# Optimization experiments

Measured on AMD Instinct MI355X. Metric: run time of the kernel, lower is better.

## Reference

```python
import jax, jax.numpy as jnp
import numpy as np

N_KERNELS = 21
N_LAYERS = 2
N_HEADS = 8
ATT_DIM = 32
FF_HID = 100
EMB = 300


def kernel_mus(n):
    mus = [1.0]
    bin_size = 2.0 / (n - 1)
    mus.append(1.0 - bin_size / 2.0)
    for _ in range(1, n - 1):
        mus.append(mus[-1] - bin_size)
    return np.array(mus, dtype=np.float32)


def kernel_sigmas(n):
    return np.array([0.001] + [0.1] * (n - 1), dtype=np.float32)


def setup_inputs() -> dict:
    key = jax.random.key(0)
    ks = jax.random.split(key, 12)
    B, LQ, LD = 32, 64, 512
    u = lambda k, s, a: jax.random.uniform(k, s, jnp.float32, -a, a)
    return dict(
        q_embed=jax.random.normal(ks[0], (B, LQ, EMB), jnp.float32),
        d_embed=jax.random.normal(ks[1], (B, LD, EMB), jnp.float32),
        mask_q=(jax.random.uniform(ks[2], (B, LQ)) > 0.1).astype(jnp.float32),
        mask_d=(jax.random.uniform(ks[3], (B, LD)) > 0.1).astype(jnp.float32),
        mixer=jnp.full((1, 1, 1), 0.5, jnp.float32),
        nn_scaler=jnp.full((1,), 0.01, jnp.float32),
        ff_w1=u(ks[4], (N_LAYERS, EMB, FF_HID), 0.05),
        ff_b1=jnp.zeros((N_LAYERS, FF_HID), jnp.float32),
        ff_w2=u(ks[5], (N_LAYERS, FF_HID, EMB), 0.05),
        ff_b2=jnp.zeros((N_LAYERS, EMB), jnp.float32),
        ln1_g=jnp.ones((N_LAYERS, EMB), jnp.float32),
        ln1_b=jnp.zeros((N_LAYERS, EMB), jnp.float32),
        att_w=u(ks[6], (N_LAYERS, EMB, 3 * ATT_DIM), 0.05),
        att_b=jnp.zeros((N_LAYERS, 3 * ATT_DIM), jnp.float32),
        out_w=u(ks[7], (N_LAYERS, ATT_DIM, EMB), 0.05),
        out_b=jnp.zeros((N_LAYERS, EMB), jnp.float32),
        ln2_g=jnp.ones((N_LAYERS, EMB), jnp.float32),
        ln2_b=jnp.zeros((N_LAYERS, EMB), jnp.float32),
        dense_w=u(ks[8], (1, N_KERNELS), 0.014),
    )


def _layer_norm(x, g, b, eps=1e-6):
    m = jnp.mean(x, -1, keepdims=True)
    s = jnp.std(x, -1, keepdims=True, ddof=1)  # torch std is unbiased
    return g * (x - m) / (s + eps) + b


def _encoder(x, mask, p):
    # AllenNLP StackedSelfAttentionEncoder: [FF -> res+LN -> MHSA -> res+LN] x2
    B, T, E = x.shape
    scale = jnp.sqrt(jnp.float32(E // N_HEADS))
    hd = ATT_DIM // N_HEADS
    for l in range(N_LAYERS):
        h = jax.nn.relu(x @ p['ff_w1'][l] + p['ff_b1'][l]) @ p['ff_w2'][l] + p['ff_b2'][l]
        h = _layer_norm(h + x, p['ln1_g'][l], p['ln1_b'][l])
        c = h @ p['att_w'][l] + p['att_b'][l]              # [B,T,3*ATT_DIM]
        q = c[..., :ATT_DIM].reshape(B, T, N_HEADS, hd)
        k = c[..., ATT_DIM:2 * ATT_DIM].reshape(B, T, N_HEADS, hd)
        v = c[..., 2 * ATT_DIM:].reshape(B, T, N_HEADS, hd)
        sims = jnp.einsum('bqhd,bkhd->bhqk', q / scale, k)
        m = mask[:, None, None, :]
        att = jax.nn.softmax(sims * m, axis=-1) * m         # AllenNLP masked_softmax
        att = att / (jnp.sum(att, -1, keepdims=True) + 1e-13)
        o = jnp.einsum('bhqk,bkhd->bqhd', att, v).reshape(B, T, ATT_DIM)
        o = o @ p['out_w'][l] + p['out_b'][l]
        x = _layer_norm(o + h, p['ln2_g'][l], p['ln2_b'][l])
    return x


def reference(q_embed, d_embed, mask_q, mask_d, mixer, nn_scaler,
              ff_w1, ff_b1, ff_w2, ff_b2, ln1_g, ln1_b,
              att_w, att_b, out_w, out_b, ln2_g, ln2_b, dense_w):
    p = dict(ff_w1=ff_w1, ff_b1=ff_b1, ff_w2=ff_w2, ff_b2=ff_b2,
             ln1_g=ln1_g, ln1_b=ln1_b, att_w=att_w, att_b=att_b,
             out_w=out_w, out_b=out_b, ln2_g=ln2_g, ln2_b=ln2_b)
    mu = jnp.asarray(kernel_mus(N_KERNELS))        # [K]
    sigma = jnp.asarray(kernel_sigmas(N_KERNELS))  # [K]
    mq = mask_q[..., None]
    md = mask_d[..., None]
    q = q_embed * mq
    d = d_embed * md
    qc = _encoder(q, mask_q, p)
    dc = _encoder(d, mask_d, p)
    q = (mixer * q + (1.0 - mixer) * qc) * mq
    d = (mixer * d + (1.0 - mixer) * dc) * md
    qd_mask = mask_q[:, :, None] * mask_d[:, None, :]  # [B,Q,D]
    qn = q / (jnp.linalg.norm(q, axis=-1, keepdims=True) + 1e-13)
    dn = d / (jnp.linalg.norm(d, axis=-1, keepdims=True) + 1e-13)
    cos = jnp.einsum('bqe,bde->bqd', qn, dn) * qd_mask
    # Gaussian RBF soft histogram: [B,Q,D,K]
    kr = jnp.exp(-(cos[..., None] - mu) ** 2 / (2.0 * sigma ** 2)) * qd_mask[..., None]
    pkq = jnp.sum(kr, axis=2)                                 # [B,Q,K]
    log_pkq = jnp.log2(jnp.clip(pkq, 1e-10)) * nn_scaler
    per_kernel = jnp.sum(log_pkq * mq, axis=1)                # [B,K]
    return jnp.squeeze(per_kernel @ dense_w.T, axis=1)        # [B]
```

## Files before the change

kernel.cpp:

```cpp
#include <hip/hip_runtime.h>
#include <hip/hip_bf16.h>

#define BATCH 32
#define LQ 64
#define LD 512
#define EMB 300
#define FFH 100
#define ATTD 32
#define NH 8
#define NK 21
#define MQ (BATCH * LQ)
#define MD (BATCH * LD)
#define MALL (MQ + MD)

typedef __attribute__((ext_vector_type(8))) short bf16x8;
typedef __attribute__((ext_vector_type(4))) float f32x4;

__device__ __forceinline__ float wave_sum(float v) {
    #pragma unroll
    for (int off = 32; off > 0; off >>= 1) v += __shfl_xor(v, off);
    return v;
}

__device__ __forceinline__ float bf2f(__hip_bfloat16 h) {
    return __bfloat162float(h);
}

__device__ __forceinline__ float4 bf4_to_f4(const __hip_bfloat16* p) {
    uint2 u = *(const uint2*)p;
    float4 f;
    f.x = __uint_as_float((u.x & 0xffffu) << 16);
    f.y = __uint_as_float(u.x & 0xffff0000u);
    f.z = __uint_as_float((u.y & 0xffffu) << 16);
    f.w = __uint_as_float(u.y & 0xffff0000u);
    return f;
}

__global__ void maskmul_all(const float* __restrict__ q_embed, const float* __restrict__ d_embed,
                            const float* __restrict__ mask_q, const float* __restrict__ mask_d,
                            __hip_bfloat16* __restrict__ xbf, float* __restrict__ mall) {
    int i = blockIdx.x * blockDim.x + threadIdx.x;
    if (i >= MALL * EMB) return;
    int tok = i / EMB;
    float m, v;
    if (tok < MQ) {
        m = mask_q[tok];
        v = q_embed[i];
    } else {
        m = mask_d[tok - MQ];
        v = d_embed[i - MQ * EMB];
    }
    xbf[i] = __float2bfloat16(v * m);
    if (i % EMB == 0) mall[tok] = m;
}

__device__ __forceinline__ void conv_seg(const float* __restrict__ w, __hip_bfloat16* __restrict__ wt,
                                         int j, int K, int N) {
    int l = j / (K * N);
    int r = j % (K * N);
    int k = r / N, n = r % N;
    wt[(size_t)l * N * K + (size_t)n * K + k] = __float2bfloat16(w[j]);
}
__global__ void convert_all(const float* __restrict__ w1, const float* __restrict__ w2,
                            const float* __restrict__ aw, const float* __restrict__ ow,
                            __hip_bfloat16* __restrict__ w1t, __hip_bfloat16* __restrict__ w2t,
                            __hip_bfloat16* __restrict__ awt, __hip_bfloat16* __restrict__ owt) {
    int i = blockIdx.x * blockDim.x + threadIdx.x;
    const int S1 = 2 * EMB * FFH;
    const int S2 = S1 + 2 * FFH * EMB;
    const int S3 = S2 + 2 * EMB * 96;
    const int S4 = S3 + 2 * ATTD * EMB;
    if (i < S1)       conv_seg(w1, w1t, i, EMB, FFH);
    else if (i < S2)  conv_seg(w2, w2t, i - S1, FFH, EMB);
    else if (i < S3)  conv_seg(aw, awt, i - S2, EMB, 96);
    else if (i < S4)  conv_seg(ow, owt, i - S3, ATTD, EMB);
}

__device__ __forceinline__ void stage_row8(const __hip_bfloat16* __restrict__ src, bool rowvalid,
                                           int K, int gk, __hip_bfloat16* dst) {
    if (rowvalid && gk + 8 <= K) {
        const uint2* p = (const uint2*)(src + gk);
        uint2 a = p[0], b = p[1];
        *(uint2*)dst = a;
        *(uint2*)(dst + 4) = b;
    } else {
        #pragma unroll
        for (int j = 0; j < 8; j++)
            dst[j] = (rowvalid && gk + j < K) ? src[gk + j] : __float2bfloat16(0.f);
    }
}

template <bool RELU>
__global__ __launch_bounds__(256) void gemm_mfma(const __hip_bfloat16* __restrict__ A,
                                                 const __hip_bfloat16* __restrict__ Bt,
                                                 const float* __restrict__ bias,
                                                 __hip_bfloat16* __restrict__ Cb,
                                                 int M, int N, int K) {
    __shared__ __align__(16) __hip_bfloat16 As[64][40];
    __shared__ __align__(16) __hip_bfloat16 Bs[64][40];
    const int tid = threadIdx.x;
    const int m0 = blockIdx.y * 64, n0 = blockIdx.x * 64;
    const int lane = tid & 63;
    const int wv = tid >> 6;
    const int wm = wv >> 1, wn = wv & 1;
    const int l15 = lane & 15, lg = lane >> 4;
    const int srow = tid >> 2, sk8 = (tid & 3) * 8;
    f32x4 acc[2][2] = {};
    const int NS = (K + 31) >> 5;
    const __hip_bfloat16* arow = A + (size_t)(m0 + srow) * K;
    const bool bvalid = (n0 + srow) < N;
    const __hip_bfloat16* brow = Bt + (size_t)(n0 + srow) * K;

    for (int s = 0; s < NS; s++) {
        const int gk = (s << 5) + sk8;
        if (s) __syncthreads();
        stage_row8(arow, true, K, gk, &As[srow][sk8]);
        stage_row8(brow, bvalid, K, gk, &Bs[srow][sk8]);
        __syncthreads();
        bf16x8 af0 = *(const bf16x8*)&As[wm * 32 + l15][lg * 8];
        bf16x8 af1 = *(const bf16x8*)&As[wm * 32 + 16 + l15][lg * 8];
        bf16x8 bf0 = *(const bf16x8*)&Bs[wn * 32 + l15][lg * 8];
        bf16x8 bf1 = *(const bf16x8*)&Bs[wn * 32 + 16 + l15][lg * 8];
        acc[0][0] = __builtin_amdgcn_mfma_f32_16x16x32_bf16(af0, bf0, acc[0][0], 0, 0, 0);
        acc[0][1] = __builtin_amdgcn_mfma_f32_16x16x32_bf16(af0, bf1, acc[0][1], 0, 0, 0);
        acc[1][0] = __builtin_amdgcn_mfma_f32_16x16x32_bf16(af1, bf0, acc[1][0], 0, 0, 0);
        acc[1][1] = __builtin_amdgcn_mfma_f32_16x16x32_bf16(af1, bf1, acc[1][1], 0, 0, 0);
    }

    #pragma unroll
    for (int fc = 0; fc < 2; fc++) {
        int col = n0 + wn * 32 + fc * 16 + l15;
        if (col >= N) continue;
        float bs = bias[col];
        #pragma unroll
        for (int fr = 0; fr < 2; fr++) {
            int rbase = m0 + wm * 32 + fr * 16 + lg * 4;
            #pragma unroll
            for (int r = 0; r < 4; r++) {
                int row = rbase + r;
                float v = acc[fr][fc][r] + bs;
                if (RELU) v = fmaxf(v, 0.f);
                Cb[(size_t)row * N + col] = __float2bfloat16(v);
            }
        }
    }
}

__global__ __launch_bounds__(256) void gemm_ln(const __hip_bfloat16* __restrict__ A,
                                               const __hip_bfloat16* __restrict__ Bt,
                                               const float* __restrict__ bias,
                                               const __hip_bfloat16* __restrict__ Res,
                                               const float* __restrict__ g,
                                               const float* __restrict__ beta,
                                               __hip_bfloat16* __restrict__ Y,
                                               int M, int K) {
    __shared__ __align__(16) __hip_bfloat16 As[32][40];
    __shared__ __align__(16) __hip_bfloat16 Bs[320][40];
    __shared__ float red[2][4][32];
    const int tid = threadIdx.x;
    const int m0 = blockIdx.x * 32;
    const int lane = tid & 63;
    const int wv = tid >> 6;
    const int l15 = lane & 15, lg = lane >> 4;
    const int c0 = wv * 80;
    f32x4 acc[2][5] = {};
    const int NS = (K + 31) >> 5;

    for (int s = 0; s < NS; s++) {
        const int gk0 = s << 5;
        if (s) __syncthreads();
        for (int ch = tid; ch < 1408; ch += 256) {
            if (ch < 128) {
                int row = ch >> 2, k8 = (ch & 3) * 8;
                stage_row8(A + (size_t)(m0 + row) * K, true, K, gk0 + k8, &As[row][k8]);
            } else {
                int cc = ch - 128;
                int row = cc >> 2, k8 = (cc & 3) * 8;
                stage_row8(Bt + (size_t)row * K, row < EMB, K, gk0 + k8, &Bs[row][k8]);
            }
        }
        __syncthreads();
        bf16x8 af[2], bfr[5];
        af[0] = *(const bf16x8*)&As[l15][lg * 8];
        af[1] = *(const bf16x8*)&As[16 + l15][lg * 8];
        #pragma unroll
        for (int fc = 0; fc < 5; fc++)
            bfr[fc] = *(const bf16x8*)&Bs[c0 + fc * 16 + l15][lg * 8];
        #pragma unroll
        for (int fr = 0; fr < 2; fr++)
            #pragma unroll
            for (int fc = 0; fc < 5; fc++)
                acc[fr][fc] = __builtin_amdgcn_mfma_f32_16x16x32_bf16(af[fr], bfr[fc], acc[fr][fc], 0, 0, 0);
    }

    float rs[2][4];
    #pragma unroll
    for (int fr = 0; fr < 2; fr++)
        #pragma unroll
        for (int r = 0; r < 4; r++) rs[fr][r] = 0.f;
    #pragma unroll
    for (int fc = 0; fc < 5; fc++) {
        int col = c0 + fc * 16 + l15;
        bool valid = col < EMB;
        float bs = valid ? bias[col] : 0.f;
        #pragma unroll
        for (int fr = 0; fr < 2; fr++) {
            int rowb = m0 + fr * 16 + lg * 4;
            #pragma unroll
            for (int r = 0; r < 4; r++) {
                float v = 0.f;
                if (valid) v = acc[fr][fc][r] + bs + bf2f(Res[(size_t)(rowb + r) * EMB + col]);
                acc[fr][fc][r] = v;
                rs[fr][r] += v;
            }
        }
    }
    #pragma unroll
    for (int fr = 0; fr < 2; fr++)
        #pragma unroll
        for (int r = 0; r < 4; r++)
            #pragma unroll
            for (int off = 1; off < 16; off <<= 1)
                rs[fr][r] += __shfl_xor(rs[fr][r], off);
    if (l15 == 0) {
        #pragma unroll
        for (int fr = 0; fr < 2; fr++)
            #pragma unroll
            for (int r = 0; r < 4; r++)
                red[0][wv][fr * 16 + lg * 4 + r] = rs[fr][r];
    }
    __syncthreads();
    float mean[2][4];
    #pragma unroll
    for (int fr = 0; fr < 2; fr++)
        #pragma unroll
        for (int r = 0; r < 4; r++) {
            int ri = fr * 16 + lg * 4 + r;
            mean[fr][r] = (red[0][0][ri] + red[0][1][ri] + red[0][2][ri] + red[0][3][ri]) * (1.f / EMB);
        }
    float rq[2][4];
    #pragma unroll
    for (int fr = 0; fr < 2; fr++)
        #pragma unroll
        for (int r = 0; r < 4; r++) rq[fr][r] = 0.f;
    #pragma unroll
    for (int fc = 0; fc < 5; fc++) {
        int col = c0 + fc * 16 + l15;
        bool valid = col < EMB;
        #pragma unroll
        for (int fr = 0; fr < 2; fr++)
            #pragma unroll
            for (int r = 0; r < 4; r++) {
                if (valid) {
                    float d = acc[fr][fc][r] - mean[fr][r];
                    rq[fr][r] += d * d;
                }
            }
    }
    #pragma unroll
    for (int fr = 0; fr < 2; fr++)
        #pragma unroll
        for (int r = 0; r < 4; r++)
            #pragma unroll
            for (int off = 1; off < 16; off <<= 1)
                rq[fr][r] += __shfl_xor(rq[fr][r], off);
    if (l15 == 0) {
        #pragma unroll
        for (int fr = 0; fr < 2; fr++)
            #pragma unroll
            for (int r = 0; r < 4; r++)
                red[1][wv][fr * 16 + lg * 4 + r] = rq[fr][r];
    }
    __syncthreads();
    float inv[2][4];
    #pragma unroll
    for (int fr = 0; fr < 2; fr++)
        #pragma unroll
        for (int r = 0; r < 4; r++) {
            int ri = fr * 16 + lg * 4 + r;
            float tot = red[1][0][ri] + red[1][1][ri] + red[1][2][ri] + red[1][3][ri];
            float stdv = sqrtf(tot * (1.f / (EMB - 1)));
            inv[fr][r] = 1.f / (stdv + 1e-6f);
        }
    #pragma unroll
    for (int fc = 0; fc < 5; fc++) {
        int col = c0 + fc * 16 + l15;
        if (col >= EMB) continue;
        float gv = g[col], bv = beta[col];
        #pragma unroll
        for (int fr = 0; fr < 2; fr++) {
            int rowb = m0 + fr * 16 + lg * 4;
            #pragma unroll
            for (int r = 0; r < 4; r++) {
                float y = gv * (acc[fr][fc][r] - mean[fr][r]) * inv[fr][r] + bv;
                Y[(size_t)(rowb + r) * EMB + col] = __float2bfloat16(y);
            }
        }
    }
}

template <int T, int RPB, int KS>
__device__ __forceinline__ void attn_body(const __hip_bfloat16* __restrict__ cseg,
                                          const float* __restrict__ mask,
                                          __hip_bfloat16* __restrict__ oseg,
                                          int bh, int rb, char* smem) {
    constexpr int BLK = 512;
    float4* Ks = (float4*)smem;
    float4* Vs = Ks + T;
    float* part = (float*)(Vs + T);
    float* nmask_s = part + RPB * 5 * (KS - 1);
    const int b = bh / NH, h = bh % NH;
    const int tid = threadIdx.x;
    const __hip_bfloat16* base = cseg + (size_t)b * T * 96;

    if (tid == 0) *nmask_s = 0.f;
    __syncthreads();
    float lnm = 0.f;
    for (int j = tid; j < T; j += BLK) {
        float m = mask[b * T + j];
        float4 kv = bf4_to_f4(base + (size_t)j * 96 + ATTD + h * 4);
        float4 vv = bf4_to_f4(base + (size_t)j * 96 + 2 * ATTD + h * 4);
        kv.x *= m; kv.y *= m; kv.z *= m; kv.w *= m;
        vv.x *= m; vv.y *= m; vv.z *= m; vv.w *= m;
        Ks[j] = kv;
        Vs[j] = vv;
        lnm += 1.f - m;
    }
    lnm = wave_sum(lnm);
    if ((tid & 63) == 0 && lnm != 0.f) atomicAdd(nmask_s, lnm);
    __syncthreads();

    const int r = rb * RPB + (tid % RPB);
    const int ks = tid / RPB;
    const float inv_scale = 0.16439898730535729f;
    float4 qv = bf4_to_f4(base + (size_t)r * 96 + h * 4);
    qv.x *= inv_scale; qv.y *= inv_scale; qv.z *= inv_scale; qv.w *= inv_scale;

    float Sall = 0.f, ox = 0.f, oy = 0.f, oz = 0.f, ow = 0.f;
    constexpr int KC = T / KS;
    const int k0 = ks * KC;
    #pragma unroll 4
    for (int k = k0; k < k0 + KC; k++) {
        float4 kv = Ks[k];
        float4 vv = Vs[k];
        float s = fmaf(qv.x, kv.x, fmaf(qv.y, kv.y, fmaf(qv.z, kv.z, qv.w * kv.w)));
        float e = __expf(s);
        Sall += e;
        ox = fmaf(e, vv.x, ox);
        oy = fmaf(e, vv.y, oy);
        oz = fmaf(e, vv.z, oz);
        ow = fmaf(e, vv.w, ow);
    }
    if (ks > 0) {
        float* p = &part[((ks - 1) * RPB + (tid % RPB)) * 5];
        p[0] = Sall; p[1] = ox; p[2] = oy; p[3] = oz; p[4] = ow;
    }
    __syncthreads();
    if (ks == 0) {
        #pragma unroll
        for (int s2 = 0; s2 < KS - 1; s2++) {
            const float* p = &part[(s2 * RPB + r - rb * RPB) * 5];
            Sall += p[0]; ox += p[1]; oy += p[2]; oz += p[3]; ow += p[4];
        }
        float Sm = Sall - *nmask_s;
        float inv = 1.f / (Sm + 1e-13f * Sall);
        __hip_bfloat16* op = oseg + (size_t)(b * T + r) * ATTD + h * 4;
        op[0] = __float2bfloat16(ox * inv);
        op[1] = __float2bfloat16(oy * inv);
        op[2] = __float2bfloat16(oz * inv);
        op[3] = __float2bfloat16(ow * inv);
    }
}

__global__ __launch_bounds__(512) void attn_both(const __hip_bfloat16* __restrict__ cbf,
                                                 const float* __restrict__ mask_q,
                                                 const float* __restrict__ mask_d,
                                                 __hip_bfloat16* __restrict__ o32) {
    __shared__ __align__(16) char smem[24576];
    int blk = blockIdx.x;
    if (blk < BATCH * NH) {
        attn_body<LQ, 64, 8>(cbf, mask_q, o32, blk, 0, smem);
    } else {
        int bid = blk - BATCH * NH;
        attn_body<LD, 128, 4>(cbf + (size_t)MQ * 96, mask_d, o32 + (size_t)MQ * ATTD,
                              bid >> 2, bid & 3, smem);
    }
}

__global__ __launch_bounds__(256) void cos_mfma(const __hip_bfloat16* __restrict__ Qn,
                                                const __hip_bfloat16* __restrict__ Dn,
                                                float* __restrict__ Cos) {
    __shared__ __align__(16) __hip_bfloat16 As[64][40];
    __shared__ __align__(16) __hip_bfloat16 Bs[64][40];
    const int b = blockIdx.y;
    const int n0 = blockIdx.x * 64;
    const int tid = threadIdx.x;
    const int lane = tid & 63;
    const int wv = tid >> 6;
    const int wm = wv >> 1, wn = wv & 1;
    const int l15 = lane & 15, lg = lane >> 4;
    const int srow = tid >> 2, sk8 = (tid & 3) * 8;
    f32x4 acc[2][2] = {};
    const int NS = (EMB + 31) >> 5;
    const __hip_bfloat16* arow = Qn + ((size_t)b * LQ + srow) * EMB;
    const __hip_bfloat16* brow = Dn + ((size_t)b * LD + n0 + srow) * EMB;

    for (int s = 0; s < NS; s++) {
        const int gk = (s << 5) + sk8;
        if (s) __syncthreads();
        stage_row8(arow, true, EMB, gk, &As[srow][sk8]);
        stage_row8(brow, true, EMB, gk, &Bs[srow][sk8]);
        __syncthreads();
        bf16x8 af0 = *(const bf16x8*)&As[wm * 32 + l15][lg * 8];
        bf16x8 af1 = *(const bf16x8*)&As[wm * 32 + 16 + l15][lg * 8];
        bf16x8 bf0 = *(const bf16x8*)&Bs[wn * 32 + l15][lg * 8];
        bf16x8 bf1 = *(const bf16x8*)&Bs[wn * 32 + 16 + l15][lg * 8];
        acc[0][0] = __builtin_amdgcn_mfma_f32_16x16x32_bf16(af0, bf0, acc[0][0], 0, 0, 0);
        acc[0][1] = __builtin_amdgcn_mfma_f32_16x16x32_bf16(af0, bf1, acc[0][1], 0, 0, 0);
        acc[1][0] = __builtin_amdgcn_mfma_f32_16x16x32_bf16(af1, bf0, acc[1][0], 0, 0, 0);
        acc[1][1] = __builtin_amdgcn_mfma_f32_16x16x32_bf16(af1, bf1, acc[1][1], 0, 0, 0);
    }

    float* cb = Cos + (size_t)b * LQ * LD;
    #pragma unroll
    for (int fc = 0; fc < 2; fc++) {
        int col = n0 + wn * 32 + fc * 16 + l15;
        #pragma unroll
        for (int fr = 0; fr < 2; fr++) {
            int rbase = wm * 32 + fr * 16 + lg * 4;
            #pragma unroll
            for (int r = 0; r < 4; r++) {
                cb[(size_t)(rbase + r) * LD + col] = acc[fr][fc][r];
            }
        }
    }
}

__global__ __launch_bounds__(256) void mixnorm_bf(const __hip_bfloat16* __restrict__ x,
                                                  const __hip_bfloat16* __restrict__ xc,
                                                  const float* __restrict__ mask,
                                                  const float* __restrict__ mixer,
                                                  __hip_bfloat16* __restrict__ out) {
    int wid = (blockIdx.x * 256 + threadIdx.x) >> 6;
    int lane = threadIdx.x & 63;
    float mixv = mixer[0];
    float mval = mask[wid];
    const __hip_bfloat16* xr = x + (size_t)wid * EMB;
    const __hip_bfloat16* xcr = xc + (size_t)wid * EMB;
    float v[5];
    float s2 = 0.f;
    #pragma unroll
    for (int r = 0; r < 5; r++) {
        int idx = lane + r * 64;
        float val = 0.f;
        if (idx < EMB) val = (mixv * bf2f(xr[idx]) + (1.f - mixv) * bf2f(xcr[idx])) * mval;
        v[r] = val;
        s2 += val * val;
    }
    s2 = wave_sum(s2);
    float inv = 1.f / (sqrtf(s2) + 1e-13f);
    __hip_bfloat16* o = out + (size_t)wid * EMB;
    #pragma unroll
    for (int r = 0; r < 5; r++) {
        int idx = lane + r * 64;
        if (idx < EMB) o[idx] = __float2bfloat16(v[r] * inv);
    }
}

__global__ __launch_bounds__(256) void pool_kernel(const float* __restrict__ Cos,
                                                   const float* __restrict__ mask_q,
                                                   const float* __restrict__ mask_d,
                                                   const float* __restrict__ nn_scaler,
                                                   float* __restrict__ lp) {
    int wid = (blockIdx.x * 256 + threadIdx.x) >> 6;
    int lane = threadIdx.x & 63;
    int b = wid >> 6, qi = wid & 63;
    const float* crow = Cos + ((size_t)b * LQ + qi) * LD;
    const float* md = mask_d + b * LD;
    float acc[NK];
    #pragma unroll
    for (int k = 0; k < NK; k++) acc[k] = 0.f;
    #pragma unroll
    for (int rr = 0; rr < LD / 64; rr++) {
        int dj = rr * 64 + lane;
        float m = md[dj];
        if (m != 0.f) {
            float cv = crow[dj];
            float d0 = cv - 1.0f;
            acc[0] += __expf(d0 * d0 * -500000.0f);
            #pragma unroll
            for (int g = 0; g < 4; g++) {
                float mu_a = 0.95f - 0.5f * g;
                float dc = cv - mu_a;
                float t = __expf(dc * dc * -50.0f);
                float r = __expf(fmaf(-10.0f, dc, -0.5f));
                #pragma unroll
                for (int j = 0; j < 5; j++) {
                    acc[1 + 5 * g + j] += t;
                    t *= r;
                    r *= 0.36787944117144233f;
                }
            }
        }
    }
    float mq = mask_q[b * LQ + qi];
    float ns = nn_scaler[0];
    #pragma unroll
    for (int k = 0; k < NK; k++) {
        float s = wave_sum(acc[k]);
        if (lane == 0) lp[((size_t)b * LQ + qi) * NK + k] = log2f(fmaxf(s, 1e-10f)) * ns * mq;
    }
}

__global__ void final_kernel(const float* __restrict__ lp, const float* __restrict__ dense_w,
                             float* __restrict__ out) {
    int b = blockIdx.x;
    int t = threadIdx.x;
    float s = 0.f;
    if (t < NK) {
        for (int qi = 0; qi < LQ; qi++) s += lp[((size_t)b * LQ + qi) * NK + t];
        s *= dense_w[t];
    }
    s = wave_sum(s);
    if (t == 0) out[b] = s;
}

extern "C" void kernel_launch(void* const* d_in, const int* in_sizes, int n_in,
                              void* d_out, int out_size, void* d_ws, size_t ws_size,
                              hipStream_t stream) {
    (void)in_sizes; (void)n_in; (void)out_size; (void)ws_size;
    const float* q_embed  = (const float*)d_in[0];
    const float* d_embed  = (const float*)d_in[1];
    const float* mask_q   = (const float*)d_in[2];
    const float* mask_d   = (const float*)d_in[3];
    const float* mixer    = (const float*)d_in[4];
    const float* nn_scaler= (const float*)d_in[5];
    const float* ff_w1    = (const float*)d_in[6];
    const float* ff_b1    = (const float*)d_in[7];
    const float* ff_w2    = (const float*)d_in[8];
    const float* ff_b2    = (const float*)d_in[9];
    const float* ln1_g    = (const float*)d_in[10];
    const float* ln1_b    = (const float*)d_in[11];
    const float* att_w    = (const float*)d_in[12];
    const float* att_b    = (const float*)d_in[13];
    const float* out_w    = (const float*)d_in[14];
    const float* out_b    = (const float*)d_in[15];
    const float* ln2_g    = (const float*)d_in[16];
    const float* ln2_b    = (const float*)d_in[17];
    const float* dense_w  = (const float*)d_in[18];
    float* out = (float*)d_out;

    float* ws   = (float*)d_ws;
    float* cosb = ws;
    float* lp   = cosb + 1048576;
    float* mall = lp + 43008;
    __hip_bfloat16* xbf   = (__hip_bfloat16*)(mall + MALL);
    __hip_bfloat16* xcbf  = xbf  + (size_t)MALL * EMB;
    __hip_bfloat16* xc2bf = xcbf + (size_t)MALL * EMB;
    __hip_bfloat16* hbf   = xc2bf + (size_t)MALL * EMB;
    __hip_bfloat16* t1bf  = hbf  + (size_t)MALL * EMB;
    __hip_bfloat16* cbf   = t1bf + (size_t)MALL * FFH;
    __hip_bfloat16* o32bf = cbf  + (size_t)MALL * 96;
    __hip_bfloat16* w1t   = o32bf + (size_t)MALL * ATTD;
    __hip_bfloat16* w2t   = w1t + 2 * FFH * EMB;
    __hip_bfloat16* awt   = w2t + 2 * EMB * FFH;
    __hip_bfloat16* owt   = awt + 2 * 96 * EMB;

    convert_all<<<(196800 + 255) / 256, 256, 0, stream>>>(ff_w1, ff_w2, att_w, out_w,
                                                          w1t, w2t, awt, owt);
    maskmul_all<<<(MALL * EMB + 255) / 256, 256, 0, stream>>>(q_embed, d_embed, mask_q, mask_d,
                                                              xbf, mall);

    const __hip_bfloat16* xcur = xbf;
    for (int l = 0; l < 2; l++) {
        __hip_bfloat16* xout = (l == 0) ? xcbf : xc2bf;
        gemm_mfma<true><<<dim3(2, MALL / 64), 256, 0, stream>>>(
            xcur, w1t + (size_t)l * FFH * EMB, ff_b1 + l * FFH, t1bf, MALL, FFH, EMB);
        gemm_ln<<<MALL / 32, 256, 0, stream>>>(
            t1bf, w2t + (size_t)l * EMB * FFH, ff_b2 + l * EMB, xcur,
            ln1_g + l * EMB, ln1_b + l * EMB, hbf, MALL, FFH);
        gemm_mfma<false><<<dim3(2, MALL / 64), 256, 0, stream>>>(
            hbf, awt + (size_t)l * 96 * EMB, att_b + l * 96, cbf, MALL, 96, EMB);
        attn_both<<<BATCH * NH + BATCH * NH * (LD / 128), 512, 0, stream>>>(
            cbf, mask_q, mask_d, o32bf);
        gemm_ln<<<MALL / 32, 256, 0, stream>>>(
            o32bf, owt + (size_t)l * EMB * ATTD, out_b + l * EMB, hbf,
            ln2_g + l * EMB, ln2_b + l * EMB, xout, MALL, ATTD);
        xcur = xout;
    }

    mixnorm_bf<<<MALL / 4, 256, 0, stream>>>(xbf, xc2bf, mall, mixer, hbf);

    cos_mfma<<<dim3(LD / 64, BATCH), 256, 0, stream>>>(hbf, hbf + (size_t)MQ * EMB, cosb);

    pool_kernel<<<(BATCH * LQ) / 4, 256, 0, stream>>>(cosb, mask_q, mask_d, nn_scaler, lp);

    final_kernel<<<BATCH, 64, 0, stream>>>(lp, dense_w, out);
}
```

Baseline: 242.5 us.

## Enlarge gemm_ln row tile to 64 and split-K the cosine GEMM

The fused GEMM+LayerNorm kernel now processes 64 rows per block instead of 32, so the 300-column weight tile staged in shared memory is reused across twice as many rows and half as many blocks are launched. The cosine-similarity GEMM is split into two K halves along a new grid dimension, each writing a separate partial buffer. The pooling kernel sums the two partials as it reads them. This raises parallelism for the small cos GEMM (256 blocks to 512) at the cost of doubled cos write/read traffic, and the gemm_ln change raises register pressure while reducing block count.

```diff
diff --git a/kernel.cpp b/kernel.cpp
--- a/kernel.cpp
+++ b/kernel.cpp
@@ -154,48 +154,50 @@
                                                const float* __restrict__ beta,
                                                __hip_bfloat16* __restrict__ Y,
                                                int M, int K) {
-    __shared__ __align__(16) __hip_bfloat16 As[32][40];
+    __shared__ __align__(16) __hip_bfloat16 As[64][40];
     __shared__ __align__(16) __hip_bfloat16 Bs[320][40];
-    __shared__ float red[2][4][32];
+    __shared__ float red[2][4][64];
     const int tid = threadIdx.x;
-    const int m0 = blockIdx.x * 32;
+    const int m0 = blockIdx.x * 64;
     const int lane = tid & 63;
     const int wv = tid >> 6;
     const int l15 = lane & 15, lg = lane >> 4;
     const int c0 = wv * 80;
-    f32x4 acc[2][5] = {};
+    f32x4 acc[4][5] = {};
     const int NS = (K + 31) >> 5;
 
     for (int s = 0; s < NS; s++) {
         const int gk0 = s << 5;
         if (s) __syncthreads();
-        for (int ch = tid; ch < 1408; ch += 256) {
-            if (ch < 128) {
+        #pragma unroll
+        for (int rnd = 0; rnd < 6; rnd++) {
+            int ch = tid + rnd * 256;
+            if (ch < 256) {
                 int row = ch >> 2, k8 = (ch & 3) * 8;
                 stage_row8(A + (size_t)(m0 + row) * K, true, K, gk0 + k8, &As[row][k8]);
             } else {
-                int cc = ch - 128;
+                int cc = ch - 256;
                 int row = cc >> 2, k8 = (cc & 3) * 8;
                 stage_row8(Bt + (size_t)row * K, row < EMB, K, gk0 + k8, &Bs[row][k8]);
             }
         }
         __syncthreads();
-        bf16x8 af[2], bfr[5];
-        af[0] = *(const bf16x8*)&As[l15][lg * 8];
-        af[1] = *(const bf16x8*)&As[16 + l15][lg * 8];
+        bf16x8 bfr[5];
         #pragma unroll
         for (int fc = 0; fc < 5; fc++)
             bfr[fc] = *(const bf16x8*)&Bs[c0 + fc * 16 + l15][lg * 8];
         #pragma unroll
-        for (int fr = 0; fr < 2; fr++)
+        for (int fr = 0; fr < 4; fr++) {
+            bf16x8 af = *(const bf16x8*)&As[fr * 16 + l15][lg * 8];
             #pragma unroll
             for (int fc = 0; fc < 5; fc++)
-                acc[fr][fc] = __builtin_amdgcn_mfma_f32_16x16x32_bf16(af[fr], bfr[fc], acc[fr][fc], 0, 0, 0);
-    }
-
-    float rs[2][4];
-    #pragma unroll
-    for (int fr = 0; fr < 2; fr++)
+                acc[fr][fc] = __builtin_amdgcn_mfma_f32_16x16x32_bf16(af, bfr[fc], acc[fr][fc], 0, 0, 0);
+        }
+    }
+
+    float rs[4][4];
+    #pragma unroll
+    for (int fr = 0; fr < 4; fr++)
         #pragma unroll
         for (int r = 0; r < 4; r++) rs[fr][r] = 0.f;
     #pragma unroll
@@ -204,7 +206,7 @@
         bool valid = col < EMB;
         float bs = valid ? bias[col] : 0.f;
         #pragma unroll
-        for (int fr = 0; fr < 2; fr++) {
+        for (int fr = 0; fr < 4; fr++) {
             int rowb = m0 + fr * 16 + lg * 4;
             #pragma unroll
             for (int r = 0; r < 4; r++) {
@@ -216,7 +218,7 @@
         }
     }
     #pragma unroll
-    for (int fr = 0; fr < 2; fr++)
+    for (int fr = 0; fr < 4; fr++)
         #pragma unroll
         for (int r = 0; r < 4; r++)
             #pragma unroll
@@ -224,23 +226,23 @@
                 rs[fr][r] += __shfl_xor(rs[fr][r], off);
     if (l15 == 0) {
         #pragma unroll
-        for (int fr = 0; fr < 2; fr++)
+        for (int fr = 0; fr < 4; fr++)
             #pragma unroll
             for (int r = 0; r < 4; r++)
                 red[0][wv][fr * 16 + lg * 4 + r] = rs[fr][r];
     }
     __syncthreads();
-    float mean[2][4];
-    #pragma unroll
-    for (int fr = 0; fr < 2; fr++)
+    float mean[4][4];
+    #pragma unroll
+    for (int fr = 0; fr < 4; fr++)
         #pragma unroll
         for (int r = 0; r < 4; r++) {
             int ri = fr * 16 + lg * 4 + r;
             mean[fr][r] = (red[0][0][ri] + red[0][1][ri] + red[0][2][ri] + red[0][3][ri]) * (1.f / EMB);
         }
-    float rq[2][4];
-    #pragma unroll
-    for (int fr = 0; fr < 2; fr++)
+    float rq[4][4];
+    #pragma unroll
+    for (int fr = 0; fr < 4; fr++)
         #pragma unroll
         for (int r = 0; r < 4; r++) rq[fr][r] = 0.f;
     #pragma unroll
@@ -248,7 +250,7 @@
         int col = c0 + fc * 16 + l15;
         bool valid = col < EMB;
         #pragma unroll
-        for (int fr = 0; fr < 2; fr++)
+        for (int fr = 0; fr < 4; fr++)
             #pragma unroll
             for (int r = 0; r < 4; r++) {
                 if (valid) {
@@ -258,7 +260,7 @@
             }
     }
     #pragma unroll
-    for (int fr = 0; fr < 2; fr++)
+    for (int fr = 0; fr < 4; fr++)
         #pragma unroll
         for (int r = 0; r < 4; r++)
             #pragma unroll
@@ -266,34 +268,26 @@
                 rq[fr][r] += __shfl_xor(rq[fr][r], off);
     if (l15 == 0) {
         #pragma unroll
-        for (int fr = 0; fr < 2; fr++)
+        for (int fr = 0; fr < 4; fr++)
             #pragma unroll
             for (int r = 0; r < 4; r++)
                 red[1][wv][fr * 16 + lg * 4 + r] = rq[fr][r];
     }
     __syncthreads();
-    float inv[2][4];
-    #pragma unroll
-    for (int fr = 0; fr < 2; fr++)
+    #pragma unroll
+    for (int fr = 0; fr < 4; fr++) {
         #pragma unroll
         for (int r = 0; r < 4; r++) {
             int ri = fr * 16 + lg * 4 + r;
             float tot = red[1][0][ri] + red[1][1][ri] + red[1][2][ri] + red[1][3][ri];
             float stdv = sqrtf(tot * (1.f / (EMB - 1)));
-            inv[fr][r] = 1.f / (stdv + 1e-6f);
-        }
-    #pragma unroll
-    for (int fc = 0; fc < 5; fc++) {
-        int col = c0 + fc * 16 + l15;
-        if (col >= EMB) continue;
-        float gv = g[col], bv = beta[col];
-        #pragma unroll
-        for (int fr = 0; fr < 2; fr++) {
-            int rowb = m0 + fr * 16 + lg * 4;
-            #pragma unroll
-            for (int r = 0; r < 4; r++) {
-                float y = gv * (acc[fr][fc][r] - mean[fr][r]) * inv[fr][r] + bv;
-                Y[(size_t)(rowb + r) * EMB + col] = __float2bfloat16(y);
+            float invv = 1.f / (stdv + 1e-6f);
+            #pragma unroll
+            for (int fc = 0; fc < 5; fc++) {
+                int col = c0 + fc * 16 + l15;
+                if (col >= EMB) continue;
+                float y = g[col] * (acc[fr][fc][r] - mean[fr][r]) * invv + beta[col];
+                Y[(size_t)(m0 + fr * 16 + lg * 4 + r) * EMB + col] = __float2bfloat16(y);
             }
         }
     }
@@ -394,6 +388,8 @@
     __shared__ __align__(16) __hip_bfloat16 Bs[64][40];
     const int b = blockIdx.y;
     const int n0 = blockIdx.x * 64;
+    const int kh = blockIdx.z;
+    const int kbeg = kh * 160;
     const int tid = threadIdx.x;
     const int lane = tid & 63;
     const int wv = tid >> 6;
@@ -401,12 +397,11 @@
     const int l15 = lane & 15, lg = lane >> 4;
     const int srow = tid >> 2, sk8 = (tid & 3) * 8;
     f32x4 acc[2][2] = {};
-    const int NS = (EMB + 31) >> 5;
     const __hip_bfloat16* arow = Qn + ((size_t)b * LQ + srow) * EMB;
     const __hip_bfloat16* brow = Dn + ((size_t)b * LD + n0 + srow) * EMB;
 
-    for (int s = 0; s < NS; s++) {
-        const int gk = (s << 5) + sk8;
+    for (int s = 0; s < 5; s++) {
+        const int gk = kbeg + (s << 5) + sk8;
         if (s) __syncthreads();
         stage_row8(arow, true, EMB, gk, &As[srow][sk8]);
         stage_row8(brow, true, EMB, gk, &Bs[srow][sk8]);
@@ -421,7 +416,7 @@
         acc[1][1] = __builtin_amdgcn_mfma_f32_16x16x32_bf16(af1, bf1, acc[1][1], 0, 0, 0);
     }
 
-    float* cb = Cos + (size_t)b * LQ * LD;
+    float* cb = Cos + (size_t)kh * (BATCH * LQ * LD) + (size_t)b * LQ * LD;
     #pragma unroll
     for (int fc = 0; fc < 2; fc++) {
         int col = n0 + wn * 32 + fc * 16 + l15;
@@ -475,7 +470,8 @@
     int wid = (blockIdx.x * 256 + threadIdx.x) >> 6;
     int lane = threadIdx.x & 63;
     int b = wid >> 6, qi = wid & 63;
-    const float* crow = Cos + ((size_t)b * LQ + qi) * LD;
+    const float* c0row = Cos + ((size_t)b * LQ + qi) * LD;
+    const float* c1row = c0row + (size_t)BATCH * LQ * LD;
     const float* md = mask_d + b * LD;
     float acc[NK];
     #pragma unroll
@@ -485,7 +481,7 @@
         int dj = rr * 64 + lane;
         float m = md[dj];
         if (m != 0.f) {
-            float cv = crow[dj];
+            float cv = c0row[dj] + c1row[dj];
             float d0 = cv - 1.0f;
             acc[0] += __expf(d0 * d0 * -500000.0f);
             #pragma unroll
@@ -552,7 +548,7 @@
 
     float* ws   = (float*)d_ws;
     float* cosb = ws;
-    float* lp   = cosb + 1048576;
+    float* lp   = cosb + 2 * 1048576;
     float* mall = lp + 43008;
     __hip_bfloat16* xbf   = (__hip_bfloat16*)(mall + MALL);
     __hip_bfloat16* xcbf  = xbf  + (size_t)MALL * EMB;
@@ -576,14 +572,14 @@
         __hip_bfloat16* xout = (l == 0) ? xcbf : xc2bf;
         gemm_mfma<true><<<dim3(2, MALL / 64), 256, 0, stream>>>(
             xcur, w1t + (size_t)l * FFH * EMB, ff_b1 + l * FFH, t1bf, MALL, FFH, EMB);
-        gemm_ln<<<MALL / 32, 256, 0, stream>>>(
+        gemm_ln<<<MALL / 64, 256, 0, stream>>>(
             t1bf, w2t + (size_t)l * EMB * FFH, ff_b2 + l * EMB, xcur,
             ln1_g + l * EMB, ln1_b + l * EMB, hbf, MALL, FFH);
         gemm_mfma<false><<<dim3(2, MALL / 64), 256, 0, stream>>>(
             hbf, awt + (size_t)l * 96 * EMB, att_b + l * 96, cbf, MALL, 96, EMB);
         attn_both<<<BATCH * NH + BATCH * NH * (LD / 128), 512, 0, stream>>>(
             cbf, mask_q, mask_d, o32bf);
-        gemm_ln<<<MALL / 32, 256, 0, stream>>>(
+        gemm_ln<<<MALL / 64, 256, 0, stream>>>(
             o32bf, owt + (size_t)l * EMB * ATTD, out_b + l * EMB, hbf,
             ln2_g + l * EMB, ln2_b + l * EMB, xout, MALL, ATTD);
         xcur = xout;
@@ -591,7 +587,7 @@
 
     mixnorm_bf<<<MALL / 4, 256, 0, stream>>>(xbf, xc2bf, mall, mixer, hbf);
 
-    cos_mfma<<<dim3(LD / 64, BATCH), 256, 0, stream>>>(hbf, hbf + (size_t)MQ * EMB, cosb);
+    cos_mfma<<<dim3(LD / 64, BATCH, 2), 256, 0, stream>>>(hbf, hbf + (size_t)MQ * EMB, cosb);
 
     pool_kernel<<<(BATCH * LQ) / 4, 256, 0, stream>>>(cosb, mask_q, mask_d, nn_scaler, lp);
 
```

After: 306.4 us. 1.26x slower.

## Stage full-K tiles in LDS once instead of per-32 K-step loop

Applied to the files above, without the earlier changes.

The GEMM, GEMM+LayerNorm and cosine kernels now load the entire K extent of their A and B tiles into shared memory in one pass, with a single barrier, and then run an unrolled MFMA loop over K. This removes the per-step barrier pairs and load-compute serialization of the old 32-wide K loop. K is made a template parameter with padded row pitch to avoid bank conflicts. The cost is much larger LDS use per block (about 84 KB for the K=300 kernels), which lowers occupancy and removes any overlap between loading and computing across blocks.

```diff
diff --git a/kernel.cpp b/kernel.cpp
--- a/kernel.cpp
+++ b/kernel.cpp
@@ -90,37 +90,41 @@
     }
 }
 
-template <bool RELU>
-__global__ __launch_bounds__(256) void gemm_mfma(const __hip_bfloat16* __restrict__ A,
+template <bool RELU, int K, int KP>
+__global__ __launch_bounds__(256) void gemm_full(const __hip_bfloat16* __restrict__ A,
                                                  const __hip_bfloat16* __restrict__ Bt,
                                                  const float* __restrict__ bias,
                                                  __hip_bfloat16* __restrict__ Cb,
-                                                 int M, int N, int K) {
-    __shared__ __align__(16) __hip_bfloat16 As[64][40];
-    __shared__ __align__(16) __hip_bfloat16 Bs[64][40];
+                                                 int N) {
+    constexpr int NC = KP / 8;
+    constexpr int NSTEP = (K + 31) / 32;
+    __shared__ __align__(16) __hip_bfloat16 As[64][KP];
+    __shared__ __align__(16) __hip_bfloat16 Bs[64][KP];
     const int tid = threadIdx.x;
     const int m0 = blockIdx.y * 64, n0 = blockIdx.x * 64;
     const int lane = tid & 63;
     const int wv = tid >> 6;
     const int wm = wv >> 1, wn = wv & 1;
     const int l15 = lane & 15, lg = lane >> 4;
-    const int srow = tid >> 2, sk8 = (tid & 3) * 8;
+
+    for (int ch = tid; ch < 2 * 64 * NC; ch += 256) {
+        int cc = (ch >= 64 * NC) ? ch - 64 * NC : ch;
+        int row = cc / NC, c = cc % NC;
+        if (ch < 64 * NC)
+            stage_row8(A + (size_t)(m0 + row) * K, true, K, c * 8, &As[row][c * 8]);
+        else
+            stage_row8(Bt + (size_t)(n0 + row) * K, (n0 + row) < N, K, c * 8, &Bs[row][c * 8]);
+    }
+    __syncthreads();
+
     f32x4 acc[2][2] = {};
-    const int NS = (K + 31) >> 5;
-    const __hip_bfloat16* arow = A + (size_t)(m0 + srow) * K;
-    const bool bvalid = (n0 + srow) < N;
-    const __hip_bfloat16* brow = Bt + (size_t)(n0 + srow) * K;
-
-    for (int s = 0; s < NS; s++) {
-        const int gk = (s << 5) + sk8;
-        if (s) __syncthreads();
-        stage_row8(arow, true, K, gk, &As[srow][sk8]);
-        stage_row8(brow, bvalid, K, gk, &Bs[srow][sk8]);
-        __syncthreads();
-        bf16x8 af0 = *(const bf16x8*)&As[wm * 32 + l15][lg * 8];
-        bf16x8 af1 = *(const bf16x8*)&As[wm * 32 + 16 + l15][lg * 8];
-        bf16x8 bf0 = *(const bf16x8*)&Bs[wn * 32 + l15][lg * 8];
-        bf16x8 bf1 = *(const bf16x8*)&Bs[wn * 32 + 16 + l15][lg * 8];
+    #pragma unroll
+    for (int ks = 0; ks < NSTEP; ks++) {
+        const int kb = ks * 32 + lg * 8;
+        bf16x8 af0 = *(const bf16x8*)&As[wm * 32 + l15][kb];
+        bf16x8 af1 = *(const bf16x8*)&As[wm * 32 + 16 + l15][kb];
+        bf16x8 bf0 = *(const bf16x8*)&Bs[wn * 32 + l15][kb];
+        bf16x8 bf1 = *(const bf16x8*)&Bs[wn * 32 + 16 + l15][kb];
         acc[0][0] = __builtin_amdgcn_mfma_f32_16x16x32_bf16(af0, bf0, acc[0][0], 0, 0, 0);
         acc[0][1] = __builtin_amdgcn_mfma_f32_16x16x32_bf16(af0, bf1, acc[0][1], 0, 0, 0);
         acc[1][0] = __builtin_amdgcn_mfma_f32_16x16x32_bf16(af1, bf0, acc[1][0], 0, 0, 0);
@@ -137,25 +141,26 @@
             int rbase = m0 + wm * 32 + fr * 16 + lg * 4;
             #pragma unroll
             for (int r = 0; r < 4; r++) {
-                int row = rbase + r;
                 float v = acc[fr][fc][r] + bs;
                 if (RELU) v = fmaxf(v, 0.f);
-                Cb[(size_t)row * N + col] = __float2bfloat16(v);
+                Cb[(size_t)(rbase + r) * N + col] = __float2bfloat16(v);
             }
         }
     }
 }
 
-__global__ __launch_bounds__(256) void gemm_ln(const __hip_bfloat16* __restrict__ A,
-                                               const __hip_bfloat16* __restrict__ Bt,
-                                               const float* __restrict__ bias,
-                                               const __hip_bfloat16* __restrict__ Res,
-                                               const float* __restrict__ g,
-                                               const float* __restrict__ beta,
-                                               __hip_bfloat16* __restrict__ Y,
-                                               int M, int K) {
-    __shared__ __align__(16) __hip_bfloat16 As[32][40];
-    __shared__ __align__(16) __hip_bfloat16 Bs[320][40];
+template <int K, int KP>
+__global__ __launch_bounds__(256) void gemm_ln_full(const __hip_bfloat16* __restrict__ A,
+                                                    const __hip_bfloat16* __restrict__ Bt,
+                                                    const float* __restrict__ bias,
+                                                    const __hip_bfloat16* __restrict__ Res,
+                                                    const float* __restrict__ g,
+                                                    const float* __restrict__ beta,
+                                                    __hip_bfloat16* __restrict__ Y) {
+    constexpr int NC = KP / 8;
+    constexpr int NSTEP = (K + 31) / 32;
+    __shared__ __align__(16) __hip_bfloat16 As[32][KP];
+    __shared__ __align__(16) __hip_bfloat16 Bs[320][KP];
     __shared__ float red[2][4][32];
     const int tid = threadIdx.x;
     const int m0 = blockIdx.x * 32;
@@ -163,34 +168,34 @@
     const int wv = tid >> 6;
     const int l15 = lane & 15, lg = lane >> 4;
     const int c0 = wv * 80;
+
+    for (int ch = tid; ch < 352 * NC; ch += 256) {
+        if (ch < 32 * NC) {
+            int row = ch / NC, c = ch % NC;
+            stage_row8(A + (size_t)(m0 + row) * K, true, K, c * 8, &As[row][c * 8]);
+        } else {
+            int cc = ch - 32 * NC;
+            int row = cc / NC, c = cc % NC;
+            stage_row8(Bt + (size_t)row * K, row < EMB, K, c * 8, &Bs[row][c * 8]);
+        }
+    }
+    __syncthreads();
+
     f32x4 acc[2][5] = {};
-    const int NS = (K + 31) >> 5;
-
-    for (int s = 0; s < NS; s++) {
-        const int gk0 = s << 5;
-        if (s) __syncthreads();
-        for (int ch = tid; ch < 1408; ch += 256) {
-            if (ch < 128) {
-                int row = ch >> 2, k8 = (ch & 3) * 8;
-                stage_row8(A + (size_t)(m0 + row) * K, true, K, gk0 + k8, &As[row][k8]);
-            } else {
-                int cc = ch - 128;
-                int row = cc >> 2, k8 = (cc & 3) * 8;
-                stage_row8(Bt + (size_t)row * K, row < EMB, K, gk0 + k8, &Bs[row][k8]);
-            }
-        }
-        __syncthreads();
-        bf16x8 af[2], bfr[5];
-        af[0] = *(const bf16x8*)&As[l15][lg * 8];
-        af[1] = *(const bf16x8*)&As[16 + l15][lg * 8];
+    #pragma unroll
+    for (int ks = 0; ks < NSTEP; ks++) {
+        const int kb = ks * 32 + lg * 8;
+        bf16x8 bfr[5];
         #pragma unroll
         for (int fc = 0; fc < 5; fc++)
-            bfr[fc] = *(const bf16x8*)&Bs[c0 + fc * 16 + l15][lg * 8];
-        #pragma unroll
-        for (int fr = 0; fr < 2; fr++)
+            bfr[fc] = *(const bf16x8*)&Bs[c0 + fc * 16 + l15][kb];
+        #pragma unroll
+        for (int fr = 0; fr < 2; fr++) {
+            bf16x8 af = *(const bf16x8*)&As[fr * 16 + l15][kb];
             #pragma unroll
             for (int fc = 0; fc < 5; fc++)
-                acc[fr][fc] = __builtin_amdgcn_mfma_f32_16x16x32_bf16(af[fr], bfr[fc], acc[fr][fc], 0, 0, 0);
+                acc[fr][fc] = __builtin_amdgcn_mfma_f32_16x16x32_bf16(af, bfr[fc], acc[fr][fc], 0, 0, 0);
+        }
     }
 
     float rs[2][4];
@@ -272,28 +277,73 @@
                 red[1][wv][fr * 16 + lg * 4 + r] = rq[fr][r];
     }
     __syncthreads();
-    float inv[2][4];
-    #pragma unroll
-    for (int fr = 0; fr < 2; fr++)
+    #pragma unroll
+    for (int fr = 0; fr < 2; fr++) {
         #pragma unroll
         for (int r = 0; r < 4; r++) {
             int ri = fr * 16 + lg * 4 + r;
             float tot = red[1][0][ri] + red[1][1][ri] + red[1][2][ri] + red[1][3][ri];
             float stdv = sqrtf(tot * (1.f / (EMB - 1)));
-            inv[fr][r] = 1.f / (stdv + 1e-6f);
-        }
-    #pragma unroll
-    for (int fc = 0; fc < 5; fc++) {
-        int col = c0 + fc * 16 + l15;
-        if (col >= EMB) continue;
-        float gv = g[col], bv = beta[col];
+            float invv = 1.f / (stdv + 1e-6f);
+            #pragma unroll
+            for (int fc = 0; fc < 5; fc++) {
+                int col = c0 + fc * 16 + l15;
+                if (col >= EMB) continue;
+                float y = g[col] * (acc[fr][fc][r] - mean[fr][r]) * invv + beta[col];
+                Y[(size_t)(m0 + fr * 16 + lg * 4 + r) * EMB + col] = __float2bfloat16(y);
+            }
+        }
+    }
+}
+
+__global__ __launch_bounds__(256) void cos_full(const __hip_bfloat16* __restrict__ Qn,
+                                                const __hip_bfloat16* __restrict__ Dn,
+                                                float* __restrict__ Cos) {
+    constexpr int KP = 328, NC = 41, NSTEP = 10;
+    __shared__ __align__(16) __hip_bfloat16 As[64][KP];
+    __shared__ __align__(16) __hip_bfloat16 Bs[64][KP];
+    const int b = blockIdx.y;
+    const int n0 = blockIdx.x * 64;
+    const int tid = threadIdx.x;
+    const int lane = tid & 63;
+    const int wv = tid >> 6;
+    const int wm = wv >> 1, wn = wv & 1;
+    const int l15 = lane & 15, lg = lane >> 4;
+    const __hip_bfloat16* Ab = Qn + (size_t)b * LQ * EMB;
+    const __hip_bfloat16* Bb = Dn + ((size_t)b * LD + n0) * EMB;
+
+    for (int ch = tid; ch < 2 * 64 * NC; ch += 256) {
+        int cc = (ch >= 64 * NC) ? ch - 64 * NC : ch;
+        int row = cc / NC, c = cc % NC;
+        if (ch < 64 * NC) stage_row8(Ab + (size_t)row * EMB, true, EMB, c * 8, &As[row][c * 8]);
+        else              stage_row8(Bb + (size_t)row * EMB, true, EMB, c * 8, &Bs[row][c * 8]);
+    }
+    __syncthreads();
+
+    f32x4 acc[2][2] = {};
+    #pragma unroll
+    for (int ks = 0; ks < NSTEP; ks++) {
+        const int kb = ks * 32 + lg * 8;
+        bf16x8 af0 = *(const bf16x8*)&As[wm * 32 + l15][kb];
+        bf16x8 af1 = *(const bf16x8*)&As[wm * 32 + 16 + l15][kb];
+        bf16x8 bf0 = *(const bf16x8*)&Bs[wn * 32 + l15][kb];
+        bf16x8 bf1 = *(const bf16x8*)&Bs[wn * 32 + 16 + l15][kb];
+        acc[0][0] = __builtin_amdgcn_mfma_f32_16x16x32_bf16(af0, bf0, acc[0][0], 0, 0, 0);
+        acc[0][1] = __builtin_amdgcn_mfma_f32_16x16x32_bf16(af0, bf1, acc[0][1], 0, 0, 0);
+        acc[1][0] = __builtin_amdgcn_mfma_f32_16x16x32_bf16(af1, bf0, acc[1][0], 0, 0, 0);
+        acc[1][1] = __builtin_amdgcn_mfma_f32_16x16x32_bf16(af1, bf1, acc[1][1], 0, 0, 0);
+    }
+
+    float* cb = Cos + (size_t)b * LQ * LD;
+    #pragma unroll
+    for (int fc = 0; fc < 2; fc++) {
+        int col = n0 + wn * 32 + fc * 16 + l15;
         #pragma unroll
         for (int fr = 0; fr < 2; fr++) {
-            int rowb = m0 + fr * 16 + lg * 4;
+            int rbase = wm * 32 + fr * 16 + lg * 4;
             #pragma unroll
             for (int r = 0; r < 4; r++) {
-                float y = gv * (acc[fr][fc][r] - mean[fr][r]) * inv[fr][r] + bv;
-                Y[(size_t)(rowb + r) * EMB + col] = __float2bfloat16(y);
+                cb[(size_t)(rbase + r) * LD + col] = acc[fr][fc][r];
             }
         }
     }
@@ -384,55 +434,6 @@
         int bid = blk - BATCH * NH;
         attn_body<LD, 128, 4>(cbf + (size_t)MQ * 96, mask_d, o32 + (size_t)MQ * ATTD,
                               bid >> 2, bid & 3, smem);
-    }
-}
-
-__global__ __launch_bounds__(256) void cos_mfma(const __hip_bfloat16* __restrict__ Qn,
-                                                const __hip_bfloat16* __restrict__ Dn,
-                                                float* __restrict__ Cos) {
-    __shared__ __align__(16) __hip_bfloat16 As[64][40];
-    __shared__ __align__(16) __hip_bfloat16 Bs[64][40];
-    const int b = blockIdx.y;
-    const int n0 = blockIdx.x * 64;
-    const int tid = threadIdx.x;
-    const int lane = tid & 63;
-    const int wv = tid >> 6;
-    const int wm = wv >> 1, wn = wv & 1;
-    const int l15 = lane & 15, lg = lane >> 4;
-    const int srow = tid >> 2, sk8 = (tid & 3) * 8;
-    f32x4 acc[2][2] = {};
-    const int NS = (EMB + 31) >> 5;
-    const __hip_bfloat16* arow = Qn + ((size_t)b * LQ + srow) * EMB;
-    const __hip_bfloat16* brow = Dn + ((size_t)b * LD + n0 + srow) * EMB;
-
-    for (int s = 0; s < NS; s++) {
-        const int gk = (s << 5) + sk8;
-        if (s) __syncthreads();
-        stage_row8(arow, true, EMB, gk, &As[srow][sk8]);
-        stage_row8(brow, true, EMB, gk, &Bs[srow][sk8]);
-        __syncthreads();
-        bf16x8 af0 = *(const bf16x8*)&As[wm * 32 + l15][lg * 8];
-        bf16x8 af1 = *(const bf16x8*)&As[wm * 32 + 16 + l15][lg * 8];
-        bf16x8 bf0 = *(const bf16x8*)&Bs[wn * 32 + l15][lg * 8];
-        bf16x8 bf1 = *(const bf16x8*)&Bs[wn * 32 + 16 + l15][lg * 8];
-        acc[0][0] = __builtin_amdgcn_mfma_f32_16x16x32_bf16(af0, bf0, acc[0][0], 0, 0, 0);
-        acc[0][1] = __builtin_amdgcn_mfma_f32_16x16x32_bf16(af0, bf1, acc[0][1], 0, 0, 0);
-        acc[1][0] = __builtin_amdgcn_mfma_f32_16x16x32_bf16(af1, bf0, acc[1][0], 0, 0, 0);
-        acc[1][1] = __builtin_amdgcn_mfma_f32_16x16x32_bf16(af1, bf1, acc[1][1], 0, 0, 0);
-    }
-
-    float* cb = Cos + (size_t)b * LQ * LD;
-    #pragma unroll
-    for (int fc = 0; fc < 2; fc++) {
-        int col = n0 + wn * 32 + fc * 16 + l15;
-        #pragma unroll
-        for (int fr = 0; fr < 2; fr++) {
-            int rbase = wm * 32 + fr * 16 + lg * 4;
-            #pragma unroll
-            for (int r = 0; r < 4; r++) {
-                cb[(size_t)(rbase + r) * LD + col] = acc[fr][fc][r];
-            }
-        }
     }
 }
 
@@ -574,24 +575,24 @@
     const __hip_bfloat16* xcur = xbf;
     for (int l = 0; l < 2; l++) {
         __hip_bfloat16* xout = (l == 0) ? xcbf : xc2bf;
-        gemm_mfma<true><<<dim3(2, MALL / 64), 256, 0, stream>>>(
-            xcur, w1t + (size_t)l * FFH * EMB, ff_b1 + l * FFH, t1bf, MALL, FFH, EMB);
-        gemm_ln<<<MALL / 32, 256, 0, stream>>>(
+        gemm_full<true, EMB, 328><<<dim3(2, MALL / 64), 256, 0, stream>>>(
+            xcur, w1t + (size_t)l * FFH * EMB, ff_b1 + l * FFH, t1bf, FFH);
+        gemm_ln_full<FFH, 136><<<MALL / 32, 256, 0, stream>>>(
             t1bf, w2t + (size_t)l * EMB * FFH, ff_b2 + l * EMB, xcur,
-            ln1_g + l * EMB, ln1_b + l * EMB, hbf, MALL, FFH);
-        gemm_mfma<false><<<dim3(2, MALL / 64), 256, 0, stream>>>(
-            hbf, awt + (size_t)l * 96 * EMB, att_b + l * 96, cbf, MALL, 96, EMB);
+            ln1_g + l * EMB, ln1_b + l * EMB, hbf);
+        gemm_full<false, EMB, 328><<<dim3(2, MALL / 64), 256, 0, stream>>>(
+            hbf, awt + (size_t)l * 96 * EMB, att_b + l * 96, cbf, 96);
         attn_both<<<BATCH * NH + BATCH * NH * (LD / 128), 512, 0, stream>>>(
             cbf, mask_q, mask_d, o32bf);
-        gemm_ln<<<MALL / 32, 256, 0, stream>>>(
+        gemm_ln_full<ATTD, 40><<<MALL / 32, 256, 0, stream>>>(
             o32bf, owt + (size_t)l * EMB * ATTD, out_b + l * EMB, hbf,
-            ln2_g + l * EMB, ln2_b + l * EMB, xout, MALL, ATTD);
+            ln2_g + l * EMB, ln2_b + l * EMB, xout);
         xcur = xout;
     }
 
     mixnorm_bf<<<MALL / 4, 256, 0, stream>>>(xbf, xc2bf, mall, mixer, hbf);
 
-    cos_mfma<<<dim3(LD / 64, BATCH), 256, 0, stream>>>(hbf, hbf + (size_t)MQ * EMB, cosb);
+    cos_full<<<dim3(LD / 64, BATCH), 256, 0, stream>>>(hbf, hbf + (size_t)MQ * EMB, cosb);
 
     pool_kernel<<<(BATCH * LQ) / 4, 256, 0, stream>>>(cosb, mask_q, mask_d, nn_scaler, lp);
 
```

New measurement: 585.8 us. 142% more time.
